# Optimization experiments

Hardware: AMD Instinct MI355X
Metric: run time of the kernel (lower is better)

The kernel has to match this reference:

```python
import jax, jax.numpy as jnp
import numpy as np
from functools import partial

P, N, C, S = 16, 128, 256, 64
HID = C // 4  # squeeze=4
NEG_SLOPE = 0.01  # nn.LeakyReLU default


def conv1d(x, w, pad):
    # x: [n, c_in, s], w: [c_out, c_in, k]
    return jax.lax.conv_general_dilated(
        x, w, window_strides=(1,), padding=[(pad, pad)],
        dimension_numbers=('NCH', 'OIH', 'NCH'))


def leaky_relu(v):
    return jnp.where(v >= 0, v, NEG_SLOPE * v)


def pool_sum(x, k):
    # x: [p, n, c, s]; sum over window k along s with symmetric padding
    return jax.lax.reduce_window(
        x, 0.0, jax.lax.add, (1, 1, 1, k), (1, 1, 1, 1),
        [(0, 0), (0, 0), (0, 0), (k // 2, k // 2)])


def pool_max(x, k):
    return jax.lax.reduce_window(
        x, -jnp.inf, jax.lax.max, (1, 1, 1, k), (1, 1, 1, 1),
        [(0, 0), (0, 0), (0, 0), (k // 2, k // 2)])


def setup_inputs() -> dict:
    key = jax.random.key(0)
    ks = jax.random.split(key, 5)
    return {
        'x': jax.random.normal(ks[0], (P, N, C, S), dtype=jnp.float32),
        'w31_a': jax.random.normal(ks[1], (P, HID, C, 3), dtype=jnp.float32) * 0.05,
        'w31_b': jax.random.normal(ks[2], (P, C, HID, 1), dtype=jnp.float32) * 0.05,
        'w33_a': jax.random.normal(ks[3], (P, HID, C, 3), dtype=jnp.float32) * 0.05,
        'w33_b': jax.random.normal(ks[4], (P, C, HID, 3), dtype=jnp.float32) * 0.05,
    }


def reference(x, w31_a, w31_b, w33_a, w33_b):
    # x: [p, n, c, s]
    # Per-part gating convs, vmapped over the part dimension p.
    def branch(xp, wa, wb, pad_b):
        h = leaky_relu(conv1d(xp, wa, 1))
        return conv1d(h, wb, pad_b)

    logits3x1 = jax.vmap(partial(branch, pad_b=0))(x, w31_a, w31_b)  # [p,n,c,s]
    logits3x3 = jax.vmap(partial(branch, pad_b=1))(x, w33_a, w33_b)  # [p,n,c,s]

    # AvgPool1d (count_include_pad=True -> divide by k) + MaxPool1d
    feat3x1 = pool_sum(x, 3) / 3.0 + pool_max(x, 3)
    feat3x3 = pool_sum(x, 5) / 5.0 + pool_max(x, 5)

    gated = feat3x1 * jax.nn.sigmoid(logits3x1) + feat3x3 * jax.nn.sigmoid(logits3x3)
    return jnp.max(gated, axis=-1)  # [p, n, c]


if __name__ == '__main__':
    out = reference(**setup_inputs())
    print(out.shape)
```

## Files before the change

### kernel.cpp

```cpp
#include <hip/hip_runtime.h>

#define PP 16
#define NN 128
#define CC 256
#define SS 64
#define HH 64

typedef __attribute__((ext_vector_type(8))) short v8bf;
typedef __attribute__((ext_vector_type(4))) float f32x4;
typedef __attribute__((ext_vector_type(4))) unsigned short u16x4;

__device__ __forceinline__ unsigned short f2bf(float f) {
    unsigned u = __float_as_uint(f);
    return (unsigned short)((u + 0x7fffu + ((u >> 16) & 1u)) >> 16);
}

__global__ void k_pack1(const float* __restrict__ w31a, const float* __restrict__ w33a,
                        unsigned short* __restrict__ wp1) {
    int u = blockIdx.x * 256 + threadIdx.x;
    int l = u & 63;
    int mi = (u >> 6) & 3;
    int kk = (u >> 8) & 7;
    int v = u >> 11;
    int t = v % 3;
    int pb = v / 3;
    int p = pb & 15, beta = pb >> 4;
    int hid = mi * 16 + (l & 15);
    int c = kk * 32 + 8 * (l >> 4);
    const float* w = (beta ? w33a : w31a) + (((size_t)(p * 64 + hid) * 256 + c) * 3 + t);
    v8bf r;
    #pragma unroll
    for (int j = 0; j < 8; ++j) r[j] = (short)f2bf(w[j * 3]);
    ((v8bf*)wp1)[u] = r;
}

__global__ void k_pack31(const float* __restrict__ w31b, unsigned short* __restrict__ wp31) {
    int u = blockIdx.x * 256 + threadIdx.x;
    int l = u & 63;
    int mt = (u >> 6) & 15;
    int kk = (u >> 10) & 1;
    int p = u >> 11;
    int cout = mt * 16 + (l & 15);
    int hid = kk * 32 + 8 * (l >> 4);
    const float* w = w31b + ((size_t)(p * 256 + cout) * 64 + hid);
    v8bf r;
    #pragma unroll
    for (int j = 0; j < 8; ++j) r[j] = (short)f2bf(w[j]);
    ((v8bf*)wp31)[u] = r;
}

__global__ void k_pack33(const float* __restrict__ w33b, unsigned short* __restrict__ wp33) {
    int u = blockIdx.x * 256 + threadIdx.x;
    int l = u & 63;
    int mt = (u >> 6) & 15;
    int kk = (u >> 10) & 1;
    int v = u >> 11;
    int t = v % 3;
    int p = v / 3;
    int cout = mt * 16 + (l & 15);
    int hid = kk * 32 + 8 * (l >> 4);
    const float* w = w33b + (((size_t)(p * 256 + cout) * 64 + hid) * 3 + t);
    v8bf r;
    #pragma unroll
    for (int j = 0; j < 8; ++j) r[j] = (short)f2bf(w[j * 3]);
    ((v8bf*)wp33)[u] = r;
}

#define XS_STRIDE 72
#define XB_OFF 73728
#define HB_OFF 107520
#define LDS_BYTES 124416

__global__ __launch_bounds__(512, 2)
void fused_mfma(const float* __restrict__ x,
                const unsigned short* __restrict__ wp1,
                const unsigned short* __restrict__ wp31,
                const unsigned short* __restrict__ wp33,
                float* __restrict__ out) {
    __shared__ __align__(16) char lds[LDS_BYTES];
    float* xs = (float*)lds;
    char* xbb = lds + XB_OFF;
    char* hbb = lds + HB_OFF;

    const int t = threadIdx.x;
    const int n = blockIdx.x, p = blockIdx.y;
    const int lane = t & 63;
    const int l15 = lane & 15, lhi = lane >> 4;
    const int w = t >> 6;

    {
        const float4* src = (const float4*)(x + (size_t)(p * NN + n) * (CC * SS));
        #pragma unroll
        for (int i = 0; i < 8; ++i) {
            int f4 = t + i * 512;
            int c = f4 >> 4, q = f4 & 15;
            float4 v = src[f4];
            *(float4*)(xs + c * XS_STRIDE + 4 + q * 4) = v;
            unsigned short b[4] = {f2bf(v.x), f2bf(v.y), f2bf(v.z), f2bf(v.w)};
            #pragma unroll
            for (int k = 0; k < 4; ++k) {
                int r = q * 4 + 1 + k;
                *(unsigned short*)(xbb + r * 512 + ((c * 2) ^ ((r & 7) << 4))) = b[k];
            }
        }
        if (t < 256) {
            *(float4*)(xs + t * XS_STRIDE) = make_float4(0.f, 0.f, 0.f, 0.f);
            *(float4*)(xs + t * XS_STRIDE + 68) = make_float4(0.f, 0.f, 0.f, 0.f);
        } else if (t < 288) {
            *(float4*)(xbb + (t - 256) * 16) = make_float4(0.f, 0.f, 0.f, 0.f);
        } else if (t < 320) {
            *(float4*)(xbb + 33280 + (t - 288) * 16) = make_float4(0.f, 0.f, 0.f, 0.f);
        } else if (t < 352) {
            int j = t - 320;
            int region = j >> 3;
            int base = (region >> 1) * 8448 + ((region & 1) ? 8320 : 0);
            *(float4*)(hbb + base + (j & 7) * 16) = make_float4(0.f, 0.f, 0.f, 0.f);
        }
    }
    __syncthreads();

    {
        const int beta = w & 1, mi = w >> 1;
        const v8bf* wv = (const v8bf*)wp1;
        v8bf A1[24];
        #pragma unroll
        for (int f = 0; f < 24; ++f) {
            int frag = ((beta * 16 + p) * 24 + f) * 4 + mi;
            A1[f] = wv[(size_t)frag * 64 + lane];
        }
        #pragma unroll
        for (int ni = 0; ni < 4; ++ni) {
            f32x4 acc = {0.f, 0.f, 0.f, 0.f};
            #pragma unroll
            for (int f = 0; f < 24; ++f) {
                int tp = f >> 3, kk = f & 7;
                int r = ni * 16 + l15 + tp;
                const v8bf* bp = (const v8bf*)(xbb + r * 512 +
                                               ((kk * 64 + 16 * lhi) ^ ((r & 7) << 4)));
                acc = __builtin_amdgcn_mfma_f32_16x16x32_bf16(A1[f], *bp, acc, 0, 0, 0);
            }
            int r2 = ni * 16 + l15 + 1;
            u16x4 hv;
            #pragma unroll
            for (int reg = 0; reg < 4; ++reg) {
                float v = acc[reg];
                v = v >= 0.f ? v : 0.01f * v;
                hv[reg] = f2bf(v);
            }
            *(u16x4*)(hbb + beta * 8448 + r2 * 128 +
                      ((mi * 32 + 8 * lhi) ^ ((r2 & 7) << 4))) = hv;
        }
    }
    __syncthreads();

    {
        const v8bf* w1v = (const v8bf*)wp31;
        const v8bf* w3v = (const v8bf*)wp33;
        v8bf A31[2][2], A33[3][2][2];
        #pragma unroll
        for (int m = 0; m < 2; ++m) {
            int mt = w * 2 + m;
            #pragma unroll
            for (int kk = 0; kk < 2; ++kk) {
                A31[kk][m] = w1v[(size_t)((p * 2 + kk) * 16 + mt) * 64 + lane];
                #pragma unroll
                for (int tp = 0; tp < 3; ++tp)
                    A33[tp][kk][m] = w3v[(size_t)(((p * 3 + tp) * 2 + kk) * 16 + mt) * 64 + lane];
            }
        }

        const size_t obase = (size_t)(p * NN + n) * CC;
        #pragma unroll
        for (int m = 0; m < 2; ++m) {
            int mt = w * 2 + m;
            float gmax[4] = {-3.4e38f, -3.4e38f, -3.4e38f, -3.4e38f};
            #pragma unroll
            for (int ni = 0; ni < 4; ++ni) {
                f32x4 a31 = {0.f, 0.f, 0.f, 0.f}, a33 = {0.f, 0.f, 0.f, 0.f};
                #pragma unroll
                for (int kk = 0; kk < 2; ++kk) {
                    int r = ni * 16 + l15 + 1;
                    const v8bf* b1 = (const v8bf*)(hbb + r * 128 +
                                                   ((kk * 64 + 16 * lhi) ^ ((r & 7) << 4)));
                    a31 = __builtin_amdgcn_mfma_f32_16x16x32_bf16(A31[kk][m], *b1, a31, 0, 0, 0);
                }
                #pragma unroll
                for (int tp = 0; tp < 3; ++tp) {
                    #pragma unroll
                    for (int kk = 0; kk < 2; ++kk) {
                        int r = ni * 16 + l15 + tp;
                        const v8bf* b3 = (const v8bf*)(hbb + 8448 + r * 128 +
                                                       ((kk * 64 + 16 * lhi) ^ ((r & 7) << 4)));
                        a33 = __builtin_amdgcn_mfma_f32_16x16x32_bf16(A33[tp][kk][m], *b3, a33, 0, 0, 0);
                    }
                }
                int s = ni * 16 + l15;
                #pragma unroll
                for (int reg = 0; reg < 4; ++reg) {
                    int c = mt * 16 + 4 * lhi + reg;
                    const float* rx = xs + c * XS_STRIDE + 4 + s;
                    float xm2 = rx[-2], xm = rx[-1], x0 = rx[0], xp = rx[1], xp2 = rx[2];
                    float s3 = (xm + x0 + xp) * (1.f / 3.f);
                    float s5 = (xm2 + xm + x0 + xp + xp2) * 0.2f;
                    float m3 = x0;
                    if (s >= 1)  m3 = fmaxf(m3, xm);
                    if (s <= 62) m3 = fmaxf(m3, xp);
                    float m5 = m3;
                    if (s >= 2)  m5 = fmaxf(m5, xm2);
                    if (s <= 61) m5 = fmaxf(m5, xp2);
                    float g = (s3 + m3) / (1.f + __expf(-a31[reg])) +
                              (s5 + m5) / (1.f + __expf(-a33[reg]));
                    gmax[reg] = fmaxf(gmax[reg], g);
                }
            }
            #pragma unroll
            for (int reg = 0; reg < 4; ++reg) {
                float g = gmax[reg];
                #pragma unroll
                for (int msk = 8; msk; msk >>= 1) g = fmaxf(g, __shfl_xor(g, msk));
                gmax[reg] = g;
            }
            if (l15 == 0) {
                float4 o = make_float4(gmax[0], gmax[1], gmax[2], gmax[3]);
                *(float4*)(out + obase + mt * 16 + 4 * lhi) = o;
            }
        }
    }
}

#define LW 72
__global__ __launch_bounds__(512, 2)
void fused_fallback(const float* __restrict__ x,
                    const float* __restrict__ w31a, const float* __restrict__ w31b,
                    const float* __restrict__ w33a, const float* __restrict__ w33b,
                    float* __restrict__ out) {
    __shared__ float lds[(CC + HH + HH) * LW];
    float* xs = lds;
    float* h31 = lds + CC * LW;
    float* h33 = h31 + HH * LW;
    const int t = threadIdx.x;
    const int n = blockIdx.x, p = blockIdx.y;
    const int lane = t & 63;
    {
        const float4* src = (const float4*)(x + (size_t)(p * NN + n) * (CC * SS));
        #pragma unroll
        for (int i = 0; i < 8; ++i) {
            int f4 = t + i * 512;
            int c = f4 >> 4, q = f4 & 15;
            *(float4*)(xs + c * LW + 4 + q * 4) = src[f4];
        }
        if (t < 256) {
            *(float4*)(xs + t * LW) = make_float4(0.f, 0.f, 0.f, 0.f);
            *(float4*)(xs + t * LW + 68) = make_float4(0.f, 0.f, 0.f, 0.f);
        } else if (t < 320) {
            int h = t - 256;
            *(float4*)(h33 + h * LW) = make_float4(0.f, 0.f, 0.f, 0.f);
            *(float4*)(h33 + h * LW + 68) = make_float4(0.f, 0.f, 0.f, 0.f);
        }
    }
    __syncthreads();
    {
        const int grp = t >> 6;
        const int conv = grp & 1;
        const int hid0 = (grp >> 1) * 16;
        const float4* wa4 = (const float4*)((conv ? w33a : w31a) + (size_t)p * (HH * CC * 3));
        float acc[16];
        #pragma unroll
        for (int h = 0; h < 16; ++h) acc[h] = 0.f;
        for (int c4 = 0; c4 < 64; ++c4) {
            float xm[4], x0[4], xp[4];
            #pragma unroll
            for (int j = 0; j < 4; ++j) {
                const float* r = xs + (c4 * 4 + j) * LW + 4 + lane;
                xm[j] = r[-1]; x0[j] = r[0]; xp[j] = r[1];
            }
            #pragma unroll
            for (int h = 0; h < 16; ++h) {
                const float4* wp = wa4 + (hid0 + h) * 192 + c4 * 3;
                float4 w0 = wp[0], w1 = wp[1], w2 = wp[2];
                float a = acc[h];
                a += xm[0]*w0.x + x0[0]*w0.y + xp[0]*w0.z;
                a += xm[1]*w0.w + x0[1]*w1.x + xp[1]*w1.y;
                a += xm[2]*w1.z + x0[2]*w1.w + xp[2]*w2.x;
                a += xm[3]*w2.y + x0[3]*w2.z + xp[3]*w2.w;
                acc[h] = a;
            }
        }
        float* dst = conv ? h33 : h31;
        #pragma unroll
        for (int h = 0; h < 16; ++h) {
            float v = acc[h];
            v = v >= 0.f ? v : 0.01f * v;
            dst[(hid0 + h) * LW + 4 + lane] = v;
        }
    }
    __syncthreads();
    {
        const int cg = t >> 6;
        const int c0 = cg * 32;
        float l31[32], l33[32];
        #pragma unroll
        for (int i = 0; i < 32; ++i) { l31[i] = 0.f; l33[i] = 0.f; }
        for (int hid = 0; hid < HH; ++hid) {
            const float* hr1 = h31 + hid * LW + 4 + lane;
            const float* hr3 = h33 + hid * LW + 4 + lane;
            float hv = hr1[0];
            float hm = hr3[-1], h0 = hr3[0], hp = hr3[1];
            #pragma unroll
            for (int i = 0; i < 32; ++i) {
                int c = c0 + i;
                l31[i] += hv * w31b[((size_t)p * 256 + c) * 64 + hid];
                const float* wb = w33b + (((size_t)p * 256 + c) * 64 + hid) * 3;
                l33[i] += hm * wb[0] + h0 * wb[1] + hp * wb[2];
            }
        }
        const size_t obase = ((size_t)p * NN + n) * CC + c0;
        #pragma unroll
        for (int i = 0; i < 32; ++i) {
            const float* r = xs + (c0 + i) * LW + 4 + lane;
            float xm2 = r[-2], xm = r[-1], x0v = r[0], xp = r[1], xp2 = r[2];
            float s3 = (xm + x0v + xp) * (1.f / 3.f);
            float s5 = (xm2 + xm + x0v + xp + xp2) * 0.2f;
            float m3 = x0v;
            if (lane >= 1)  m3 = fmaxf(m3, xm);
            if (lane <= 62) m3 = fmaxf(m3, xp);
            float m5 = m3;
            if (lane >= 2)  m5 = fmaxf(m5, xm2);
            if (lane <= 61) m5 = fmaxf(m5, xp2);
            float g = (s3 + m3) / (1.f + __expf(-l31[i])) + (s5 + m5) / (1.f + __expf(-l33[i]));
            #pragma unroll
            for (int off = 32; off; off >>= 1)
                g = fmaxf(g, __shfl_xor(g, off));
            if (lane == 0) out[obase + i] = g;
        }
    }
}

extern "C" void kernel_launch(void* const* d_in, const int* in_sizes, int n_in,
                              void* d_out, int out_size, void* d_ws, size_t ws_size,
                              hipStream_t stream) {
    const float* x    = (const float*)d_in[0];
    const float* w31a = (const float*)d_in[1];
    const float* w31b = (const float*)d_in[2];
    const float* w33a = (const float*)d_in[3];
    const float* w33b = (const float*)d_in[4];
    float* out = (float*)d_out;

    const size_t need = 5242880;
    dim3 grid(NN, PP);
    if (ws_size >= need) {
        unsigned short* wp1  = (unsigned short*)d_ws;
        unsigned short* wp31 = (unsigned short*)((char*)d_ws + 3145728);
        unsigned short* wp33 = (unsigned short*)((char*)d_ws + 3670016);
        k_pack1 <<<768, 256, 0, stream>>>(w31a, w33a, wp1);
        k_pack31<<<128, 256, 0, stream>>>(w31b, wp31);
        k_pack33<<<384, 256, 0, stream>>>(w33b, wp33);
        fused_mfma<<<grid, 512, 0, stream>>>(x, wp1, wp31, wp33, out);
    } else {
        fused_fallback<<<grid, 512, 0, stream>>>(x, w31a, w31b, w33a, w33b, out);
    }
}
```

Measured before the change: 303.6 us.

## Switch to 32x32 MFMA tiles, drop fp32 x copy, raise occupancy

The fused kernel moves from 16x16x32 to 32x32x16 bf16 MFMA tiles, with new weight packing layouts and pack kernels that read weights using vectorized float4 loads. It drops the fp32 copy of x in LDS and computes the pooling features from the bf16 transposed tile instead, shrinking LDS from about 124 KB to about 52 KB. Launch bounds go from 2 to 6 blocks per CU. The transpose into bf16 is staged through a temp buffer in chunks, and the sigmoid divide becomes a reciprocal. Computing the pooling from bf16 x lowers accuracy of the pooled features, and the chunked staging adds extra barriers.

```diff
diff --git a/kernel.cpp b/kernel.cpp
--- a/kernel.cpp
+++ b/kernel.cpp
@@ -7,7 +7,7 @@
 #define HH 64
 
 typedef __attribute__((ext_vector_type(8))) short v8bf;
-typedef __attribute__((ext_vector_type(4))) float f32x4;
+typedef __attribute__((ext_vector_type(16))) float f32x16;
 typedef __attribute__((ext_vector_type(4))) unsigned short u16x4;
 
 __device__ __forceinline__ unsigned short f2bf(float f) {
@@ -18,188 +18,213 @@
 __global__ void k_pack1(const float* __restrict__ w31a, const float* __restrict__ w33a,
                         unsigned short* __restrict__ wp1) {
     int u = blockIdx.x * 256 + threadIdx.x;
-    int l = u & 63;
-    int mi = (u >> 6) & 3;
-    int kk = (u >> 8) & 7;
-    int v = u >> 11;
-    int t = v % 3;
-    int pb = v / 3;
-    int p = pb & 15, beta = pb >> 4;
-    int hid = mi * 16 + (l & 15);
-    int c = kk * 32 + 8 * (l >> 4);
-    const float* w = (beta ? w33a : w31a) + (((size_t)(p * 64 + hid) * 256 + c) * 3 + t);
-    v8bf r;
-    #pragma unroll
-    for (int j = 0; j < 8; ++j) r[j] = (short)f2bf(w[j * 3]);
-    ((v8bf*)wp1)[u] = r;
+    int lane = u & 63;
+    int ks   = (u >> 6) & 15;
+    int mi   = (u >> 10) & 1;
+    int p    = (u >> 11) & 15;
+    int beta = u >> 15;
+    int hid = mi * 32 + (lane & 31);
+    int c0  = ks * 16 + 8 * (lane >> 5);
+    const float* src = (beta ? w33a : w31a) + ((size_t)(p * 64 + hid) * 256 + c0) * 3;
+    float f[24];
+    #pragma unroll
+    for (int i = 0; i < 6; ++i) *(float4*)(f + i * 4) = ((const float4*)src)[i];
+    v8bf* dst = (v8bf*)wp1;
+    #pragma unroll
+    for (int tp = 0; tp < 3; ++tp) {
+        v8bf r;
+        #pragma unroll
+        for (int j = 0; j < 8; ++j) r[j] = (short)f2bf(f[j * 3 + tp]);
+        dst[(size_t)((((beta * 16 + p) * 3 + tp) * 16 + ks) * 2 + mi) * 64 + lane] = r;
+    }
 }
 
 __global__ void k_pack31(const float* __restrict__ w31b, unsigned short* __restrict__ wp31) {
     int u = blockIdx.x * 256 + threadIdx.x;
-    int l = u & 63;
-    int mt = (u >> 6) & 15;
-    int kk = (u >> 10) & 1;
-    int p = u >> 11;
-    int cout = mt * 16 + (l & 15);
-    int hid = kk * 32 + 8 * (l >> 4);
-    const float* w = w31b + ((size_t)(p * 256 + cout) * 64 + hid);
+    int lane = u & 63;
+    int ct = (u >> 6) & 7;
+    int ks = (u >> 9) & 3;
+    int p  = u >> 11;
+    int cout = ct * 32 + (lane & 31);
+    int hid0 = ks * 16 + 8 * (lane >> 5);
+    const float* src = w31b + (size_t)(p * 256 + cout) * 64 + hid0;
+    float f[8];
+    *(float4*)(f)     = ((const float4*)src)[0];
+    *(float4*)(f + 4) = ((const float4*)src)[1];
     v8bf r;
     #pragma unroll
-    for (int j = 0; j < 8; ++j) r[j] = (short)f2bf(w[j]);
-    ((v8bf*)wp31)[u] = r;
+    for (int j = 0; j < 8; ++j) r[j] = (short)f2bf(f[j]);
+    ((v8bf*)wp31)[(size_t)((p * 4 + ks) * 8 + ct) * 64 + lane] = r;
 }
 
 __global__ void k_pack33(const float* __restrict__ w33b, unsigned short* __restrict__ wp33) {
     int u = blockIdx.x * 256 + threadIdx.x;
-    int l = u & 63;
-    int mt = (u >> 6) & 15;
-    int kk = (u >> 10) & 1;
-    int v = u >> 11;
-    int t = v % 3;
-    int p = v / 3;
-    int cout = mt * 16 + (l & 15);
-    int hid = kk * 32 + 8 * (l >> 4);
-    const float* w = w33b + (((size_t)(p * 256 + cout) * 64 + hid) * 3 + t);
-    v8bf r;
-    #pragma unroll
-    for (int j = 0; j < 8; ++j) r[j] = (short)f2bf(w[j * 3]);
-    ((v8bf*)wp33)[u] = r;
-}
-
-#define XS_STRIDE 72
-#define XB_OFF 73728
-#define HB_OFF 107520
-#define LDS_BYTES 124416
-
-__global__ __launch_bounds__(512, 2)
+    int lane = u & 63;
+    int ct = (u >> 6) & 7;
+    int ks = (u >> 9) & 3;
+    int p  = u >> 11;
+    int cout = ct * 32 + (lane & 31);
+    int hid0 = ks * 16 + 8 * (lane >> 5);
+    const float* src = w33b + ((size_t)(p * 256 + cout) * 64 + hid0) * 3;
+    float f[24];
+    #pragma unroll
+    for (int i = 0; i < 6; ++i) *(float4*)(f + i * 4) = ((const float4*)src)[i];
+    v8bf* dst = (v8bf*)wp33;
+    #pragma unroll
+    for (int tp = 0; tp < 3; ++tp) {
+        v8bf r;
+        #pragma unroll
+        for (int j = 0; j < 8; ++j) r[j] = (short)f2bf(f[j * 3 + tp]);
+        dst[(size_t)(((p * 3 + tp) * 4 + ks) * 8 + ct) * 64 + lane] = r;
+    }
+}
+
+#define XB_ROWB 512
+#define HB_OFF 34816
+#define HB_BR 8448
+#define LDS_BYTES 51712
+
+__global__ __launch_bounds__(512, 6)
 void fused_mfma(const float* __restrict__ x,
                 const unsigned short* __restrict__ wp1,
                 const unsigned short* __restrict__ wp31,
                 const unsigned short* __restrict__ wp33,
                 float* __restrict__ out) {
     __shared__ __align__(16) char lds[LDS_BYTES];
-    float* xs = (float*)lds;
-    char* xbb = lds + XB_OFF;
-    char* hbb = lds + HB_OFF;
+    char* xb = lds;
+    char* hb = lds + HB_OFF;
+    float* tmp = (float*)(lds + HB_OFF);
 
     const int t = threadIdx.x;
     const int n = blockIdx.x, p = blockIdx.y;
+    const int pn = p * NN + n;
     const int lane = t & 63;
-    const int l15 = lane & 15, lhi = lane >> 4;
+    const int l31 = lane & 31, lhi5 = lane >> 5;
     const int w = t >> 6;
-
-    {
-        const float4* src = (const float4*)(x + (size_t)(p * NN + n) * (CC * SS));
-        #pragma unroll
-        for (int i = 0; i < 8; ++i) {
-            int f4 = t + i * 512;
-            int c = f4 >> 4, q = f4 & 15;
-            float4 v = src[f4];
-            *(float4*)(xs + c * XS_STRIDE + 4 + q * 4) = v;
-            unsigned short b[4] = {f2bf(v.x), f2bf(v.y), f2bf(v.z), f2bf(v.w)};
-            #pragma unroll
-            for (int k = 0; k < 4; ++k) {
-                int r = q * 4 + 1 + k;
-                *(unsigned short*)(xbb + r * 512 + ((c * 2) ^ ((r & 7) << 4))) = b[k];
-            }
-        }
-        if (t < 256) {
-            *(float4*)(xs + t * XS_STRIDE) = make_float4(0.f, 0.f, 0.f, 0.f);
-            *(float4*)(xs + t * XS_STRIDE + 68) = make_float4(0.f, 0.f, 0.f, 0.f);
-        } else if (t < 288) {
-            *(float4*)(xbb + (t - 256) * 16) = make_float4(0.f, 0.f, 0.f, 0.f);
-        } else if (t < 320) {
-            *(float4*)(xbb + 33280 + (t - 288) * 16) = make_float4(0.f, 0.f, 0.f, 0.f);
-        } else if (t < 352) {
-            int j = t - 320;
-            int region = j >> 3;
-            int base = (region >> 1) * 8448 + ((region & 1) ? 8320 : 0);
-            *(float4*)(hbb + base + (j & 7) * 16) = make_float4(0.f, 0.f, 0.f, 0.f);
+    const float4 z4 = make_float4(0.f, 0.f, 0.f, 0.f);
+
+    if (t < 128) {
+        int rr = t >> 5;
+        int row = (rr < 2) ? rr : 64 + rr;
+        *(float4*)(xb + row * XB_ROWB + (t & 31) * 16) = z4;
+    }
+
+    const float4* xsrc = (const float4*)x + (size_t)pn * 4096;
+    for (int ch = 0; ch < 4; ++ch) {
+        #pragma unroll
+        for (int i = 0; i < 2; ++i) {
+            int j = t + i * 512;
+            *(float4*)((char*)tmp + j * 16) = xsrc[ch * 1024 + j];
+        }
+        __syncthreads();
+        {
+            int s = t & 63, cg = t >> 6;
+            unsigned short b[8];
+            #pragma unroll
+            for (int k2 = 0; k2 < 8; ++k2) b[k2] = f2bf(tmp[(cg * 8 + k2) * 64 + s]);
+            int row = s + 2;
+            int col = (2 * (ch * 64 + cg * 8)) ^ ((row & 7) << 4);
+            v8bf vv;
+            #pragma unroll
+            for (int k2 = 0; k2 < 8; ++k2) vv[k2] = (short)b[k2];
+            *(v8bf*)(xb + row * XB_ROWB + col) = vv;
+        }
+        __syncthreads();
+    }
+
+    if (t < 32) {
+        int br = t >> 4;
+        int row = ((t >> 3) & 1) ? 65 : 0;
+        *(float4*)(hb + br * HB_BR + row * 128 + (t & 7) * 16) = z4;
+    }
+
+    {
+        const int beta = w & 1, mi = (w >> 1) & 1, ni = (w >> 2) & 1;
+        const v8bf* wv = (const v8bf*)wp1;
+        const size_t abase = (size_t)((beta * 16 + p) * 3) * 32 * 64 + (size_t)mi * 64 + lane;
+        f32x16 acc = {};
+        #pragma unroll
+        for (int tp = 0; tp < 3; ++tp) {
+            int r = ni * 32 + l31 + tp + 1;
+            int swz = (r & 7) << 4;
+            const char* xrow = xb + r * XB_ROWB;
+            #pragma unroll
+            for (int ks = 0; ks < 16; ++ks) {
+                v8bf A = wv[abase + (size_t)(tp * 16 + ks) * 128];
+                v8bf B = *(const v8bf*)(xrow + ((2 * (ks * 16 + 8 * lhi5)) ^ swz));
+                acc = __builtin_amdgcn_mfma_f32_32x32x16_bf16(A, B, acc, 0, 0, 0);
+            }
+        }
+        int r2 = ni * 32 + l31 + 1;
+        int swz2 = (r2 & 7) << 4;
+        char* hrow = hb + beta * HB_BR + r2 * 128;
+        #pragma unroll
+        for (int rg = 0; rg < 4; ++rg) {
+            int hid0 = mi * 32 + 8 * rg + 4 * lhi5;
+            u16x4 hv;
+            #pragma unroll
+            for (int q = 0; q < 4; ++q) {
+                float v = acc[rg * 4 + q];
+                v = v >= 0.f ? v : 0.01f * v;
+                hv[q] = f2bf(v);
+            }
+            *(u16x4*)(hrow + ((2 * hid0) ^ swz2)) = hv;
         }
     }
     __syncthreads();
 
     {
-        const int beta = w & 1, mi = w >> 1;
-        const v8bf* wv = (const v8bf*)wp1;
-        v8bf A1[24];
-        #pragma unroll
-        for (int f = 0; f < 24; ++f) {
-            int frag = ((beta * 16 + p) * 24 + f) * 4 + mi;
-            A1[f] = wv[(size_t)frag * 64 + lane];
-        }
-        #pragma unroll
-        for (int ni = 0; ni < 4; ++ni) {
-            f32x4 acc = {0.f, 0.f, 0.f, 0.f};
-            #pragma unroll
-            for (int f = 0; f < 24; ++f) {
-                int tp = f >> 3, kk = f & 7;
-                int r = ni * 16 + l15 + tp;
-                const v8bf* bp = (const v8bf*)(xbb + r * 512 +
-                                               ((kk * 64 + 16 * lhi) ^ ((r & 7) << 4)));
-                acc = __builtin_amdgcn_mfma_f32_16x16x32_bf16(A1[f], *bp, acc, 0, 0, 0);
-            }
-            int r2 = ni * 16 + l15 + 1;
-            u16x4 hv;
-            #pragma unroll
-            for (int reg = 0; reg < 4; ++reg) {
-                float v = acc[reg];
-                v = v >= 0.f ? v : 0.01f * v;
-                hv[reg] = f2bf(v);
-            }
-            *(u16x4*)(hbb + beta * 8448 + r2 * 128 +
-                      ((mi * 32 + 8 * lhi) ^ ((r2 & 7) << 4))) = hv;
-        }
-    }
-    __syncthreads();
-
-    {
+        const int ct = w;
         const v8bf* w1v = (const v8bf*)wp31;
         const v8bf* w3v = (const v8bf*)wp33;
-        v8bf A31[2][2], A33[3][2][2];
-        #pragma unroll
-        for (int m = 0; m < 2; ++m) {
-            int mt = w * 2 + m;
-            #pragma unroll
-            for (int kk = 0; kk < 2; ++kk) {
-                A31[kk][m] = w1v[(size_t)((p * 2 + kk) * 16 + mt) * 64 + lane];
+        float gm[16];
+        #pragma unroll
+        for (int i = 0; i < 16; ++i) gm[i] = -3.4e38f;
+
+        #pragma unroll
+        for (int ni = 0; ni < 2; ++ni) {
+            const int s = ni * 32 + l31;
+            f32x16 a31 = {};
+            {
+                int r = s + 1;
+                int swz = (r & 7) << 4;
+                const char* hrow = hb + r * 128;
                 #pragma unroll
-                for (int tp = 0; tp < 3; ++tp)
-                    A33[tp][kk][m] = w3v[(size_t)(((p * 3 + tp) * 2 + kk) * 16 + mt) * 64 + lane];
-            }
-        }
-
-        const size_t obase = (size_t)(p * NN + n) * CC;
-        #pragma unroll
-        for (int m = 0; m < 2; ++m) {
-            int mt = w * 2 + m;
-            float gmax[4] = {-3.4e38f, -3.4e38f, -3.4e38f, -3.4e38f};
-            #pragma unroll
-            for (int ni = 0; ni < 4; ++ni) {
-                f32x4 a31 = {0.f, 0.f, 0.f, 0.f}, a33 = {0.f, 0.f, 0.f, 0.f};
+                for (int ks = 0; ks < 4; ++ks) {
+                    v8bf A = w1v[(size_t)((p * 4 + ks) * 8 + ct) * 64 + lane];
+                    v8bf B = *(const v8bf*)(hrow + ((2 * (ks * 16 + 8 * lhi5)) ^ swz));
+                    a31 = __builtin_amdgcn_mfma_f32_32x32x16_bf16(A, B, a31, 0, 0, 0);
+                }
+            }
+            f32x16 a33 = {};
+            #pragma unroll
+            for (int tp = 0; tp < 3; ++tp) {
+                int r = s + tp;
+                int swz = (r & 7) << 4;
+                const char* hrow = hb + HB_BR + r * 128;
                 #pragma unroll
-                for (int kk = 0; kk < 2; ++kk) {
-                    int r = ni * 16 + l15 + 1;
-                    const v8bf* b1 = (const v8bf*)(hbb + r * 128 +
-                                                   ((kk * 64 + 16 * lhi) ^ ((r & 7) << 4)));
-                    a31 = __builtin_amdgcn_mfma_f32_16x16x32_bf16(A31[kk][m], *b1, a31, 0, 0, 0);
+                for (int ks = 0; ks < 4; ++ks) {
+                    v8bf A = w3v[(size_t)(((p * 3 + tp) * 4 + ks) * 8 + ct) * 64 + lane];
+                    v8bf B = *(const v8bf*)(hrow + ((2 * (ks * 16 + 8 * lhi5)) ^ swz));
+                    a33 = __builtin_amdgcn_mfma_f32_32x32x16_bf16(A, B, a33, 0, 0, 0);
+                }
+            }
+            #pragma unroll
+            for (int rg = 0; rg < 4; ++rg) {
+                int c0 = ct * 32 + 8 * rg + 4 * lhi5;
+                float q[5][4];
+                #pragma unroll
+                for (int d = 0; d < 5; ++d) {
+                    int r = s + d;
+                    u16x4 hv = *(const u16x4*)(xb + r * XB_ROWB + ((2 * c0) ^ ((r & 7) << 4)));
+                    #pragma unroll
+                    for (int qi = 0; qi < 4; ++qi)
+                        q[d][qi] = __uint_as_float((unsigned)hv[qi] << 16);
                 }
                 #pragma unroll
-                for (int tp = 0; tp < 3; ++tp) {
-                    #pragma unroll
-                    for (int kk = 0; kk < 2; ++kk) {
-                        int r = ni * 16 + l15 + tp;
-                        const v8bf* b3 = (const v8bf*)(hbb + 8448 + r * 128 +
-                                                       ((kk * 64 + 16 * lhi) ^ ((r & 7) << 4)));
-                        a33 = __builtin_amdgcn_mfma_f32_16x16x32_bf16(A33[tp][kk][m], *b3, a33, 0, 0, 0);
-                    }
-                }
-                int s = ni * 16 + l15;
-                #pragma unroll
-                for (int reg = 0; reg < 4; ++reg) {
-                    int c = mt * 16 + 4 * lhi + reg;
-                    const float* rx = xs + c * XS_STRIDE + 4 + s;
-                    float xm2 = rx[-2], xm = rx[-1], x0 = rx[0], xp = rx[1], xp2 = rx[2];
+                for (int qi = 0; qi < 4; ++qi) {
+                    int reg = rg * 4 + qi;
+                    float xm2 = q[0][qi], xm = q[1][qi], x0 = q[2][qi], xp = q[3][qi], xp2 = q[4][qi];
                     float s3 = (xm + x0 + xp) * (1.f / 3.f);
                     float s5 = (xm2 + xm + x0 + xp + xp2) * 0.2f;
                     float m3 = x0;
@@ -208,21 +233,26 @@
                     float m5 = m3;
                     if (s >= 2)  m5 = fmaxf(m5, xm2);
                     if (s <= 61) m5 = fmaxf(m5, xp2);
-                    float g = (s3 + m3) / (1.f + __expf(-a31[reg])) +
-                              (s5 + m5) / (1.f + __expf(-a33[reg]));
-                    gmax[reg] = fmaxf(gmax[reg], g);
+                    float s31 = __builtin_amdgcn_rcpf(1.f + __expf(-a31[reg]));
+                    float s33 = __builtin_amdgcn_rcpf(1.f + __expf(-a33[reg]));
+                    float g = (s3 + m3) * s31 + (s5 + m5) * s33;
+                    gm[reg] = fmaxf(gm[reg], g);
                 }
             }
-            #pragma unroll
-            for (int reg = 0; reg < 4; ++reg) {
-                float g = gmax[reg];
-                #pragma unroll
-                for (int msk = 8; msk; msk >>= 1) g = fmaxf(g, __shfl_xor(g, msk));
-                gmax[reg] = g;
-            }
-            if (l15 == 0) {
-                float4 o = make_float4(gmax[0], gmax[1], gmax[2], gmax[3]);
-                *(float4*)(out + obase + mt * 16 + 4 * lhi) = o;
+        }
+        #pragma unroll
+        for (int reg = 0; reg < 16; ++reg) {
+            float g = gm[reg];
+            #pragma unroll
+            for (int off = 16; off; off >>= 1) g = fmaxf(g, __shfl_xor(g, off));
+            gm[reg] = g;
+        }
+        if (l31 == 0) {
+            float* ob = out + (size_t)pn * 256 + ct * 32 + 4 * lhi5;
+            #pragma unroll
+            for (int rg = 0; rg < 4; ++rg) {
+                float4 o = make_float4(gm[rg * 4], gm[rg * 4 + 1], gm[rg * 4 + 2], gm[rg * 4 + 3]);
+                *(float4*)(ob + 8 * rg) = o;
             }
         }
     }
@@ -352,9 +382,9 @@
         unsigned short* wp1  = (unsigned short*)d_ws;
         unsigned short* wp31 = (unsigned short*)((char*)d_ws + 3145728);
         unsigned short* wp33 = (unsigned short*)((char*)d_ws + 3670016);
-        k_pack1 <<<768, 256, 0, stream>>>(w31a, w33a, wp1);
+        k_pack1 <<<256, 256, 0, stream>>>(w31a, w33a, wp1);
         k_pack31<<<128, 256, 0, stream>>>(w31b, wp31);
-        k_pack33<<<384, 256, 0, stream>>>(w33b, wp33);
+        k_pack33<<<128, 256, 0, stream>>>(w33b, wp33);
         fused_mfma<<<grid, 512, 0, stream>>>(x, wp1, wp31, wp33, out);
     } else {
         fused_fallback<<<grid, 512, 0, stream>>>(x, w31a, w31b, w33a, w33b, out);
```

New measurement: 454.3 us. 49.6% more time.
